# Kernel tuning notes

Measured on AMD Instinct MI355X. Metric: run time of the kernel, lower is better.

Reference implementation:

```python
import jax, jax.numpy as jnp
import numpy as np

GROUP_SIZE = 64
BITS = 4
VALS_PER_WORD = 32 // BITS  # 8 nibbles per uint32


def setup_inputs() -> dict:
    key = jax.random.key(0)
    ks = jax.random.split(key, 7)
    B, S, I, O = 4, 2048, 4096, 4096
    G = I // GROUP_SIZE
    x = jax.random.normal(ks[0], (B, S, I), dtype=jnp.float32)
    channel_scale = jax.random.uniform(ks[1], (1, 1, I), dtype=jnp.float32, minval=0.5, maxval=1.5)
    # packed int4 weights: random uint32 words
    qweight = jax.random.randint(ks[2], (O, I // VALS_PER_WORD), 0, 2147483647, dtype=jnp.int32).astype(jnp.uint32)
    q_perm = jax.random.permutation(ks[3], I).astype(jnp.int32)
    scales = jax.random.uniform(ks[4], (O, G), dtype=jnp.float32, minval=0.001, maxval=0.02)
    zeros = jax.random.normal(ks[5], (O, G), dtype=jnp.float32) * 0.05
    bias = jax.random.normal(ks[6], (O,), dtype=jnp.float32) * 0.02
    return {"x": x, "channel_scale": channel_scale, "qweight": qweight,
            "q_perm": q_perm, "scales": scales, "zeros": zeros, "bias": bias}


def _dequantize(qweight, scales, zeros):
    # qweight: (O, I/8) uint32 -> nibbles little-endian within each word
    O, packed = qweight.shape
    shifts = (jnp.arange(VALS_PER_WORD, dtype=jnp.uint32) * BITS)  # (8,)
    wq = (qweight[:, :, None] >> shifts[None, None, :]) & jnp.uint32((1 << BITS) - 1)
    wq = wq.reshape(O, packed * VALS_PER_WORD).astype(jnp.float32)  # (O, I)
    # mlx dequantize: w = wq * scale + bias(zeros), per group of GROUP_SIZE along input dim
    s = jnp.repeat(scales, GROUP_SIZE, axis=1)  # (O, I)
    z = jnp.repeat(zeros, GROUP_SIZE, axis=1)   # (O, I)
    return wq * s + z


def reference(x, channel_scale, qweight, q_perm, scales, zeros, bias):
    # per-channel scale
    x = x * channel_scale
    # optional permute gather along feature axis
    x = jnp.take(x, q_perm, axis=-1)
    # group-wise int4 dequant matmul (transpose=True: out = x @ W^T)
    W = _dequantize(qweight, scales, zeros)  # (O, I)
    out = jnp.einsum('bsi,oi->bso', x, W)
    return out + bias
```

## Files before the change

kernel.cpp:

```cpp
#include <hip/hip_runtime.h>
#include <hip/hip_bf16.h>

typedef unsigned short u16;
typedef unsigned int u32;
typedef unsigned char u8;

#define M_DIM 8192
#define K_DIM 4096
#define N_DIM 4096
#define GROUPS 64

typedef int intx4 __attribute__((ext_vector_type(4)));

__device__ __forceinline__ void gload_lds16(const void* g, void* l) {
  __builtin_amdgcn_global_load_lds(
      (const __attribute__((address_space(1))) void*)g,
      (__attribute__((address_space(3))) void*)l, 16, 0, 0);
}

__device__ __forceinline__ float block_absmax(float amax, float* red) {
#pragma unroll
  for (int off = 32; off; off >>= 1)
    amax = fmaxf(amax, __shfl_xor(amax, off, 64));
  const int wave = threadIdx.x >> 6;
  if ((threadIdx.x & 63) == 0) red[wave] = amax;
  __syncthreads();
  return fmaxf(fmaxf(red[0], red[1]), fmaxf(red[2], red[3]));
}

__device__ __forceinline__ u32 pack4(const float* v, float inv) {
  u32 r = 0;
#pragma unroll
  for (int i = 0; i < 4; ++i) {
    int q = (int)__builtin_rintf(v[i] * inv);
    q = q > 127 ? 127 : (q < -127 ? -127 : q);
    r |= ((u32)(u8)(char)q) << (8 * i);
  }
  return r;
}

__global__ __launch_bounds__(256) void prep_x(
    const float* __restrict__ x, const float* __restrict__ cs,
    u8* __restrict__ xq, float* __restrict__ sx) {
  __shared__ float red[4];
  const size_t m = blockIdx.x;
  const float* xr = x + m * K_DIM;
  const int base = threadIdx.x * 16;
  float v[16];
  float amax = 0.f;
#pragma unroll
  for (int j = 0; j < 4; ++j) {
    float4 xv = *(const float4*)(xr + base + j * 4);
    float4 cv = *(const float4*)(cs + base + j * 4);
    v[j * 4 + 0] = xv.x * cv.x;
    v[j * 4 + 1] = xv.y * cv.y;
    v[j * 4 + 2] = xv.z * cv.z;
    v[j * 4 + 3] = xv.w * cv.w;
#pragma unroll
    for (int i = 0; i < 4; ++i) amax = fmaxf(amax, fabsf(v[j * 4 + i]));
  }
  amax = block_absmax(amax, red);
  amax = fmaxf(amax, 1e-20f);
  const float inv = 127.0f / amax;
  uint4 p;
  p.x = pack4(v + 0, inv);
  p.y = pack4(v + 4, inv);
  p.z = pack4(v + 8, inv);
  p.w = pack4(v + 12, inv);
  *(uint4*)(xq + m * K_DIM + base) = p;
  if (threadIdx.x == 0) sx[m] = amax * (1.0f / 127.0f);
}

__global__ __launch_bounds__(256) void prep_w(
    const u32* __restrict__ qw, const int* __restrict__ perm,
    const float* __restrict__ scales, const float* __restrict__ zeros,
    u8* __restrict__ wq, float* __restrict__ sw) {
  __shared__ float rowbuf[K_DIM];
  __shared__ float red[4];
  const int o = blockIdx.x;
  const u32* qrow = qw + (size_t)o * (K_DIM / 8);
  float amax = 0.f;
#pragma unroll
  for (int it = 0; it < 2; ++it) {
    int t = it * 256 + threadIdx.x;
    u32 q = qrow[t];
    int g = t >> 3;
    float s = scales[o * GROUPS + g];
    float z = zeros[o * GROUPS + g];
#pragma unroll
    for (int n = 0; n < 8; ++n) {
      float v = (float)((q >> (4 * n)) & 15u) * s + z;
      amax = fmaxf(amax, fabsf(v));
      rowbuf[perm[t * 8 + n]] = v;
    }
  }
  __syncthreads();
  amax = block_absmax(amax, red);
  amax = fmaxf(amax, 1e-20f);
  const float inv = 127.0f / amax;
  const int base = threadIdx.x * 16;
  uint4 p;
  p.x = pack4(rowbuf + base + 0, inv);
  p.y = pack4(rowbuf + base + 4, inv);
  p.z = pack4(rowbuf + base + 8, inv);
  p.w = pack4(rowbuf + base + 12, inv);
  *(uint4*)(wq + (size_t)o * K_DIM + base) = p;
  if (threadIdx.x == 0) sw[o] = amax * (1.0f / 127.0f);
}

__global__ __launch_bounds__(256) void gemm_i8(
    const u8* __restrict__ A, const u8* __restrict__ B,
    const float* __restrict__ sx, const float* __restrict__ sw,
    const float* __restrict__ bias, float* __restrict__ out) {
  __shared__ __align__(16) u8 As[128 * 64];
  __shared__ __align__(16) u8 Bs[128 * 64];
  const int tid = threadIdx.x;
  const int lane = tid & 63;
  const int wave = tid >> 6;
  const int wm = wave >> 1, wn = wave & 1;
  const int q = lane >> 4, lr = lane & 15;
  const int qs = q ^ ((lr >> 1) & 3);
  const int blockN = blockIdx.x * 128;
  const int blockM = blockIdx.y * 128;

  intx4 acc[4][4];
#pragma unroll
  for (int i = 0; i < 4; ++i)
#pragma unroll
    for (int j = 0; j < 4; ++j) acc[i][j] = (intx4)0;

  const char* Abase = (const char*)(A + (size_t)blockM * K_DIM);
  const char* Bbase = (const char*)(B + (size_t)blockN * K_DIM);

  const int c0 = tid, c1 = 256 + tid;
  const int r0 = c0 >> 2, kc0 = (c0 & 3) ^ ((c0 >> 3) & 3);
  const int r1 = c1 >> 2, kc1 = (c1 & 3) ^ ((c1 >> 3) & 3);

  for (int kt = 0; kt < K_DIM / 64; ++kt) {
    const size_t koff = (size_t)kt * 64;
    gload_lds16(Abase + (size_t)r0 * K_DIM + koff + kc0 * 16, &As[c0 * 16]);
    gload_lds16(Abase + (size_t)r1 * K_DIM + koff + kc1 * 16, &As[c1 * 16]);
    gload_lds16(Bbase + (size_t)r0 * K_DIM + koff + kc0 * 16, &Bs[c0 * 16]);
    gload_lds16(Bbase + (size_t)r1 * K_DIM + koff + kc1 * 16, &Bs[c1 * 16]);
    __syncthreads();

    intx4 af[4], bfr[4];
#pragma unroll
    for (int mi = 0; mi < 4; ++mi)
      af[mi] = *(const intx4*)&As[(wm * 64 + mi * 16 + lr) * 64 + qs * 16];
#pragma unroll
    for (int ni = 0; ni < 4; ++ni)
      bfr[ni] = *(const intx4*)&Bs[(wn * 64 + ni * 16 + lr) * 64 + qs * 16];
#pragma unroll
    for (int mi = 0; mi < 4; ++mi)
#pragma unroll
      for (int ni = 0; ni < 4; ++ni)
        acc[mi][ni] = __builtin_amdgcn_mfma_i32_16x16x64_i8(
            af[mi], bfr[ni], acc[mi][ni], 0, 0, 0);
    __syncthreads();
  }

#pragma unroll
  for (int ni = 0; ni < 4; ++ni) {
    const int col = blockN + wn * 64 + ni * 16 + lr;
    const float swv = sw[col];
    const float bv = bias[col];
#pragma unroll
    for (int mi = 0; mi < 4; ++mi) {
      const int row0 = blockM + wm * 64 + mi * 16 + q * 4;
#pragma unroll
      for (int r = 0; r < 4; ++r) {
        const float s = sx[row0 + r] * swv;
        out[(size_t)(row0 + r) * N_DIM + col] = (float)acc[mi][ni][r] * s + bv;
      }
    }
  }
}

extern "C" void kernel_launch(void* const* d_in, const int* in_sizes, int n_in,
                              void* d_out, int out_size, void* d_ws, size_t ws_size,
                              hipStream_t stream) {
  const float* x      = (const float*)d_in[0];
  const float* cs     = (const float*)d_in[1];
  const u32*   qw     = (const u32*)d_in[2];
  const int*   perm   = (const int*)d_in[3];
  const float* scales = (const float*)d_in[4];
  const float* zeros  = (const float*)d_in[5];
  const float* bias   = (const float*)d_in[6];
  float* out = (float*)d_out;

  u8* xq = (u8*)d_ws;
  u8* wq = xq + (size_t)M_DIM * K_DIM;
  float* sx = (float*)(wq + (size_t)N_DIM * K_DIM);
  float* sw = sx + M_DIM;

  hipLaunchKernelGGL(prep_x, dim3(M_DIM), dim3(256), 0, stream, x, cs, xq, sx);
  hipLaunchKernelGGL(prep_w, dim3(N_DIM), dim3(256), 0, stream,
                     qw, perm, scales, zeros, wq, sw);
  hipLaunchKernelGGL(gemm_i8, dim3(N_DIM / 128, M_DIM / 128), dim3(256), 0,
                     stream, xq, wq, sx, sw, bias, out);
}
```

Before: 408.1 us.

## Enlarge GEMM tile to 256x256 with triple-buffered LDS prefetch pipeline

Grows the int8 GEMM block tile from 128x128 to 256x256, using 512 threads in a 2x4 wave grid where each wave computes 128x64. It adds a three-stage LDS ring buffer fed by async global-to-LDS loads, so one barrier per k-step replaces two and loads overlap with MFMA work. MFMA sections are raised in priority with s_setprio. In exchange the kernel uses 96KB of LDS and 128 accumulator registers per lane, which limits occupancy, and correctness depends on the hand-written vmcnt waits.

```diff
diff --git a/kernel.cpp b/kernel.cpp
--- a/kernel.cpp
+++ b/kernel.cpp
@@ -108,57 +108,83 @@
   if (threadIdx.x == 0) sw[o] = amax * (1.0f / 127.0f);
 }
 
-__global__ __launch_bounds__(256) void gemm_i8(
+#define BM 256
+#define BN 256
+#define BK 64
+#define KTILES (K_DIM / BK)
+
+__global__ __launch_bounds__(512, 2) void gemm_i8(
     const u8* __restrict__ A, const u8* __restrict__ B,
     const float* __restrict__ sx, const float* __restrict__ sw,
     const float* __restrict__ bias, float* __restrict__ out) {
-  __shared__ __align__(16) u8 As[128 * 64];
-  __shared__ __align__(16) u8 Bs[128 * 64];
+  __shared__ __align__(16) u8 As[3][BM * BK];
+  __shared__ __align__(16) u8 Bs[3][BN * BK];
   const int tid = threadIdx.x;
   const int lane = tid & 63;
   const int wave = tid >> 6;
-  const int wm = wave >> 1, wn = wave & 1;
+  const int wm = wave >> 2;
+  const int wn = wave & 3;
   const int q = lane >> 4, lr = lane & 15;
   const int qs = q ^ ((lr >> 1) & 3);
-  const int blockN = blockIdx.x * 128;
-  const int blockM = blockIdx.y * 128;
-
-  intx4 acc[4][4];
-#pragma unroll
-  for (int i = 0; i < 4; ++i)
-#pragma unroll
-    for (int j = 0; j < 4; ++j) acc[i][j] = (intx4)0;
+  const int blockN = blockIdx.x * BN;
+  const int blockM = blockIdx.y * BM;
 
   const char* Abase = (const char*)(A + (size_t)blockM * K_DIM);
   const char* Bbase = (const char*)(B + (size_t)blockN * K_DIM);
 
-  const int c0 = tid, c1 = 256 + tid;
+  const int c0 = tid, c1 = tid + 512;
   const int r0 = c0 >> 2, kc0 = (c0 & 3) ^ ((c0 >> 3) & 3);
   const int r1 = c1 >> 2, kc1 = (c1 & 3) ^ ((c1 >> 3) & 3);
 
-  for (int kt = 0; kt < K_DIM / 64; ++kt) {
-    const size_t koff = (size_t)kt * 64;
-    gload_lds16(Abase + (size_t)r0 * K_DIM + koff + kc0 * 16, &As[c0 * 16]);
-    gload_lds16(Abase + (size_t)r1 * K_DIM + koff + kc1 * 16, &As[c1 * 16]);
-    gload_lds16(Bbase + (size_t)r0 * K_DIM + koff + kc0 * 16, &Bs[c0 * 16]);
-    gload_lds16(Bbase + (size_t)r1 * K_DIM + koff + kc1 * 16, &Bs[c1 * 16]);
-    __syncthreads();
-
-    intx4 af[4], bfr[4];
-#pragma unroll
-    for (int mi = 0; mi < 4; ++mi)
-      af[mi] = *(const intx4*)&As[(wm * 64 + mi * 16 + lr) * 64 + qs * 16];
+  intx4 acc[8][4];
+#pragma unroll
+  for (int i = 0; i < 8; ++i)
+#pragma unroll
+    for (int j = 0; j < 4; ++j) acc[i][j] = (intx4)0;
+
+  auto stage = [&](int t, int b) {
+    const size_t koff = (size_t)t * BK;
+    gload_lds16(Abase + (size_t)r0 * K_DIM + koff + kc0 * 16, &As[b][c0 * 16]);
+    gload_lds16(Abase + (size_t)r1 * K_DIM + koff + kc1 * 16, &As[b][c1 * 16]);
+    gload_lds16(Bbase + (size_t)r0 * K_DIM + koff + kc0 * 16, &Bs[b][c0 * 16]);
+    gload_lds16(Bbase + (size_t)r1 * K_DIM + koff + kc1 * 16, &Bs[b][c1 * 16]);
+  };
+
+  auto compute = [&](int b) {
+    intx4 af[8], bf[4];
+#pragma unroll
+    for (int mi = 0; mi < 8; ++mi)
+      af[mi] = *(const intx4*)&As[b][(wm * 128 + mi * 16 + lr) * 64 + qs * 16];
 #pragma unroll
     for (int ni = 0; ni < 4; ++ni)
-      bfr[ni] = *(const intx4*)&Bs[(wn * 64 + ni * 16 + lr) * 64 + qs * 16];
-#pragma unroll
-    for (int mi = 0; mi < 4; ++mi)
+      bf[ni] = *(const intx4*)&Bs[b][(wn * 64 + ni * 16 + lr) * 64 + qs * 16];
+    __builtin_amdgcn_s_setprio(1);
+#pragma unroll
+    for (int mi = 0; mi < 8; ++mi)
 #pragma unroll
       for (int ni = 0; ni < 4; ++ni)
         acc[mi][ni] = __builtin_amdgcn_mfma_i32_16x16x64_i8(
-            af[mi], bfr[ni], acc[mi][ni], 0, 0, 0);
-    __syncthreads();
-  }
+            af[mi], bf[ni], acc[mi][ni], 0, 0, 0);
+    __builtin_amdgcn_s_setprio(0);
+  };
+
+  stage(0, 0);
+  stage(1, 1);
+  asm volatile("s_waitcnt vmcnt(4)\n\ts_barrier" ::: "memory");
+
+  int bc = 0;
+  int bs = 2;
+  for (int t = 0; t < KTILES - 2; ++t) {
+    stage(t + 2, bs);
+    compute(bc);
+    asm volatile("s_waitcnt vmcnt(4)\n\ts_barrier" ::: "memory");
+    bc = (bc == 2) ? 0 : bc + 1;
+    bs = (bs == 2) ? 0 : bs + 1;
+  }
+  compute(bc);
+  asm volatile("s_waitcnt vmcnt(0)\n\ts_barrier" ::: "memory");
+  bc = (bc == 2) ? 0 : bc + 1;
+  compute(bc);
 
 #pragma unroll
   for (int ni = 0; ni < 4; ++ni) {
@@ -166,8 +192,8 @@
     const float swv = sw[col];
     const float bv = bias[col];
 #pragma unroll
-    for (int mi = 0; mi < 4; ++mi) {
-      const int row0 = blockM + wm * 64 + mi * 16 + q * 4;
+    for (int mi = 0; mi < 8; ++mi) {
+      const int row0 = blockM + wm * 128 + mi * 16 + q * 4;
 #pragma unroll
       for (int r = 0; r < 4; ++r) {
         const float s = sx[row0 + r] * swv;
@@ -197,6 +223,6 @@
   hipLaunchKernelGGL(prep_x, dim3(M_DIM), dim3(256), 0, stream, x, cs, xq, sx);
   hipLaunchKernelGGL(prep_w, dim3(N_DIM), dim3(256), 0, stream,
                      qw, perm, scales, zeros, wq, sw);
-  hipLaunchKernelGGL(gemm_i8, dim3(N_DIM / 128, M_DIM / 128), dim3(256), 0,
+  hipLaunchKernelGGL(gemm_i8, dim3(N_DIM / BN, M_DIM / BM), dim3(512), 0,
                      stream, xq, wq, sx, sw, bias, out);
 }
```

Result: slower. 420.7 us (+3.1%).
